# Optimization experiments

Hardware: AMD Instinct MI355X
Metric: run time of the kernel (lower is better)

## Reference

```python
import jax, jax.numpy as jnp
import numpy as np

IN, H, NCLS = 1280, 128, 263


def _lstm_scan(x_tbd, Wih, Whh, bih, bhh):
    # x_tbd: [T, B, IN]; PyTorch gate order: i, f, g, o. Wih: [4H, IN], Whh: [4H, H]
    B = x_tbd.shape[1]
    b = bih + bhh
    # precompute input projections once: [T, B, 4H]
    xp = jnp.einsum('tbd,gd->tbg', x_tbd, Wih) + b

    def step(carry, xg):
        h, c = carry
        gates = xg + h @ Whh.T
        i, f, g, o = jnp.split(gates, 4, axis=-1)
        i = jax.nn.sigmoid(i)
        f = jax.nn.sigmoid(f)
        g = jnp.tanh(g)
        o = jax.nn.sigmoid(o)
        c = f * c + i * g
        h = o * jnp.tanh(c)
        return (h, c), h

    h0 = jnp.zeros((B, H), x_tbd.dtype)
    c0 = jnp.zeros((B, H), x_tbd.dtype)
    _, hs = jax.lax.scan(step, (h0, c0), xp)
    return hs  # [T, B, H]


def setup_inputs() -> dict:
    key = jax.random.key(0)
    ks = jax.random.split(key, 11)
    s_ih = 1.0 / np.sqrt(H)
    u = lambda k, shape: jax.random.uniform(k, shape, jnp.float32, -s_ih, s_ih)
    return {
        'x': jax.random.normal(ks[0], (64, 512, IN), jnp.float32),
        'Wih_f': u(ks[1], (4 * H, IN)),
        'Whh_f': u(ks[2], (4 * H, H)),
        'bih_f': u(ks[3], (4 * H,)),
        'bhh_f': u(ks[4], (4 * H,)),
        'Wih_b': u(ks[5], (4 * H, IN)),
        'Whh_b': u(ks[6], (4 * H, H)),
        'bih_b': u(ks[7], (4 * H,)),
        'bhh_b': u(ks[8], (4 * H,)),
        'W1': u(ks[9], (NCLS, 2 * H)),
        'b1': u(ks[10], (NCLS,)),
    }


def reference(x, Wih_f, Whh_f, bih_f, bhh_f, Wih_b, Whh_b, bih_b, bhh_b, W1, b1):
    x_tbd = jnp.swapaxes(x, 0, 1)  # [T, B, IN]
    h_f = _lstm_scan(x_tbd, Wih_f, Whh_f, bih_f, bhh_f)           # [T, B, H]
    h_b = _lstm_scan(x_tbd[::-1], Wih_b, Whh_b, bih_b, bhh_b)[::-1]
    h = jnp.concatenate([h_f, h_b], axis=-1)  # [T, B, 2H]
    pooled = jnp.max(h, axis=0)               # temporal max-pool -> [B, 2H]
    # dropout treated as identity (deterministic eval-mode baseline)
    return pooled @ W1.T + b1                  # [B, 263]
```

## Files before the change

kernel.cpp:

```cpp
#include <hip/hip_runtime.h>
#include <hip/hip_bf16.h>

typedef short short8v __attribute__((ext_vector_type(8)));
typedef short short4v __attribute__((ext_vector_type(4)));
typedef float f32x4v __attribute__((ext_vector_type(4)));

#define T_LEN 512
#define BATCH 64
#define INDIM 1280
#define HDIM 128
#define G4 512
#define NCOLS 1024
#define NCLS 263

typedef __attribute__((address_space(1))) const void gvoid_t;
typedef __attribute__((address_space(3))) void lvoid_t;
#define GLOAD_LDS16(g, l) __builtin_amdgcn_global_load_lds((gvoid_t*)(g), (lvoid_t*)(l), 16, 0, 0)

static __device__ __forceinline__ short f2bf(float f) {
    union { float f; unsigned u; } v; v.f = f;
    unsigned r = v.u + 0x7FFF + ((v.u >> 16) & 1);
    return (short)(r >> 16);
}

__global__ void convert_x_kernel(const float4* __restrict__ x, short4v* __restrict__ out, int n4) {
    int i = blockIdx.x * blockDim.x + threadIdx.x;
    int stride = gridDim.x * blockDim.x;
    for (; i < n4; i += stride) {
        float4 v = x[i];
        short4v o;
        o[0] = f2bf(v.x); o[1] = f2bf(v.y); o[2] = f2bf(v.z); o[3] = f2bf(v.w);
        out[i] = o;
    }
}

__global__ void convert_w_kernel(const float* __restrict__ Wf, const float* __restrict__ Wb,
                                 const float* __restrict__ bihf, const float* __restrict__ bhhf,
                                 const float* __restrict__ bihb, const float* __restrict__ bhhb,
                                 short* __restrict__ wout, float* __restrict__ biasc) {
    int i = blockIdx.x * blockDim.x + threadIdx.x;
    int stride = gridDim.x * blockDim.x;
    const int n4 = (G4 * INDIM) / 4;
    for (int k = i; k < 2 * n4; k += stride) {
        const float4* src = (k < n4) ? (const float4*)Wf : (const float4*)Wb;
        float4 v = src[(k < n4) ? k : (k - n4)];
        short4v o;
        o[0] = f2bf(v.x); o[1] = f2bf(v.y); o[2] = f2bf(v.z); o[3] = f2bf(v.w);
        ((short4v*)wout)[k] = o;
    }
    if (i < NCOLS)
        biasc[i] = (i < G4) ? (bihf[i] + bhhf[i]) : (bihb[i - G4] + bhhb[i - G4]);
}

#define BM 128
#define BN 128
#define BK 32

__global__ __launch_bounds__(256) void gemm_xp_kernel(const short* __restrict__ A,
                                                      const short* __restrict__ Bw,
                                                      const float* __restrict__ bias,
                                                      float* __restrict__ C) {
    __shared__ __align__(16) short As[BM * BK];
    __shared__ __align__(16) short Bs[BN * BK];
    const int tid = threadIdx.x;
    const int w = tid >> 6;
    const int l = tid & 63;
    const int bm = blockIdx.x * BM;
    const int bn = blockIdx.y * BN;
    const int wm = (w >> 1) * 64;
    const int wn = (w & 1) * 64;
    const int lr = l & 15;
    const int lk = (l >> 4) * 8;

    f32x4v acc[4][4];
#pragma unroll
    for (int m = 0; m < 4; m++)
#pragma unroll
        for (int n = 0; n < 4; n++) acc[m][n] = (f32x4v)0.0f;

    const int srow = tid >> 2;
    const int scol = (tid & 3) * 8;

#pragma unroll
    for (int i = 0; i < 2; i++) {
        GLOAD_LDS16(A + (long)(bm + i * 64 + srow) * INDIM + scol, &As[(i * 64 + (w << 4)) * BK]);
        GLOAD_LDS16(Bw + (long)(bn + i * 64 + srow) * INDIM + scol, &Bs[(i * 64 + (w << 4)) * BK]);
    }

    for (int k0 = 0; k0 < INDIM; k0 += BK) {
        __syncthreads();
        short8v af[4], bf[4];
#pragma unroll
        for (int m = 0; m < 4; m++) af[m] = *(const short8v*)&As[(wm + m * 16 + lr) * BK + lk];
#pragma unroll
        for (int n = 0; n < 4; n++) bf[n] = *(const short8v*)&Bs[(wn + n * 16 + lr) * BK + lk];
        __syncthreads();
        if (k0 + BK < INDIM) {
            const int k1 = k0 + BK;
#pragma unroll
            for (int i = 0; i < 2; i++) {
                GLOAD_LDS16(A + (long)(bm + i * 64 + srow) * INDIM + k1 + scol, &As[(i * 64 + (w << 4)) * BK]);
                GLOAD_LDS16(Bw + (long)(bn + i * 64 + srow) * INDIM + k1 + scol, &Bs[(i * 64 + (w << 4)) * BK]);
            }
        }
#pragma unroll
        for (int m = 0; m < 4; m++)
#pragma unroll
            for (int n = 0; n < 4; n++)
                acc[m][n] = __builtin_amdgcn_mfma_f32_16x16x32_bf16(af[m], bf[n], acc[m][n], 0, 0, 0);
    }

#pragma unroll
    for (int m = 0; m < 4; m++) {
        const int row = bm + wm + m * 16 + (l >> 4) * 4;
#pragma unroll
        for (int n = 0; n < 4; n++) {
            const int col = bn + wn + n * 16 + lr;
            const float bv = bias[col];
#pragma unroll
            for (int r = 0; r < 4; r++)
                C[(long)(row + r) * NCOLS + col] = acc[m][n][r] + bv;
        }
    }
}

__global__ __launch_bounds__(256, 1) void lstm_rec_kernel(const float* __restrict__ xp,
                                                          const float* __restrict__ Whh_f,
                                                          const float* __restrict__ Whh_b,
                                                          float* __restrict__ pooled) {
    __shared__ __align__(16) short hbf[2][3][136];
    __shared__ __align__(16) float glds[4][2][136];

    const int bid = blockIdx.x;
    const int d = bid & 1;
    const int b0 = (bid >> 1) * 2;
    const int tid = threadIdx.x;
    const int w = tid >> 6;
    const int l = tid & 63;
    const int lr = l & 15;
    const int lg = l >> 4;
    const int lk = lg * 8;
    const int hrow = lr < 2 ? lr : 2;

    const float* __restrict__ Whh = d ? Whh_b : Whh_f;

    short8v afragW[8][4];
#pragma unroll
    for (int nt = 0; nt < 8; nt++) {
        const int gc = w * 128 + nt * 16 + lr;
#pragma unroll
        for (int kk = 0; kk < 4; kk++) {
            const float* src = Whh + gc * HDIM + kk * 32 + lk;
            short8v f;
#pragma unroll
            for (int j = 0; j < 8; j++) f[j] = f2bf(src[j]);
            afragW[nt][kk] = f;
        }
    }

    for (int i = tid; i < 2 * 3 * 136; i += 256) ((short*)hbf)[i] = 0;

    const int eb = tid >> 7;
    const int ec = tid & 127;
    const float* xbase = xp + (long)(b0 + eb) * T_LEN * NCOLS + d * G4 + ec;

    float c = 0.0f;
    float hmax = -1e30f;

#define LOADXV(tq, dst) { \
    int tt_ = d ? (T_LEN - 1 - (tq)) : (tq); \
    tt_ = tt_ < 0 ? 0 : (tt_ > T_LEN - 1 ? T_LEN - 1 : tt_); \
    const float* p_ = xbase + (long)tt_ * NCOLS; \
    _Pragma("unroll") for (int nt_ = 0; nt_ < 4; nt_++) \
        dst[nt_] = p_[nt_ * 128]; \
}

    float xvA[4], xvB[4];
    LOADXV(0, xvA);
    LOADXV(1, xvB);

    __syncthreads();

#define L2E 1.44269504088896f

#define STEP(t, pb, xv) { \
    short8v hfrag[4]; \
    _Pragma("unroll") for (int kk = 0; kk < 4; kk++) \
        hfrag[kk] = *(const short8v*)&hbf[pb][hrow][kk * 32 + lk]; \
    _Pragma("unroll") for (int nt = 0; nt < 8; nt++) { \
        f32x4v a = (f32x4v)0.0f; \
        _Pragma("unroll") for (int kk = 0; kk < 4; kk++) \
            a = __builtin_amdgcn_mfma_f32_16x16x32_bf16(afragW[nt][kk], hfrag[kk], a, 0, 0, 0); \
        if (lr < 2) *(f32x4v*)&glds[w][lr][nt * 16 + lg * 4] = a; \
    } \
    asm volatile("s_waitcnt lgkmcnt(0)\n\ts_barrier" ::: "memory"); \
    { \
        float gi = glds[0][eb][ec] + xv[0]; \
        float gf = glds[1][eb][ec] + xv[1]; \
        float gg = glds[2][eb][ec] + xv[2]; \
        float go = glds[3][eb][ec] + xv[3]; \
        float ea = __builtin_amdgcn_exp2f(-gi * L2E); \
        float eb_ = __builtin_amdgcn_exp2f(-gf * L2E); \
        float pa = 1.0f + ea, pbv = 1.0f + eb_; \
        float inv1 = __builtin_amdgcn_rcpf(pa * pbv); \
        float si = pbv * inv1; \
        float sf = pa * inv1; \
        float eg = __builtin_amdgcn_exp2f(gg * (2.0f * L2E)); \
        float eo = __builtin_amdgcn_exp2f(-go * L2E); \
        float pg = 1.0f + eg, po = 1.0f + eo; \
        float inv2 = __builtin_amdgcn_rcpf(pg * po); \
        float tg = 1.0f - 2.0f * po * inv2; \
        float so = pg * inv2; \
        c = sf * c + si * tg; \
        float ecx = __builtin_amdgcn_exp2f(c * (2.0f * L2E)); \
        float tc = 1.0f - 2.0f * __builtin_amdgcn_rcpf(1.0f + ecx); \
        float h = so * tc; \
        hmax = fmaxf(hmax, h); \
        hbf[(pb) ^ 1][eb][ec] = f2bf(h); \
    } \
    LOADXV((t) + 2, xv); \
    asm volatile("s_waitcnt lgkmcnt(0)\n\ts_barrier" ::: "memory"); \
}

    for (int t = 0; t < T_LEN; t += 2) {
        STEP(t, 0, xvA);
        STEP(t + 1, 1, xvB);
    }

    pooled[(b0 + eb) * 256 + d * 128 + ec] = hmax;
#undef STEP
#undef LOADXV
}

__global__ void logits_kernel(const float* __restrict__ pooled, const float* __restrict__ W1,
                              const float* __restrict__ b1, float* __restrict__ out) {
    __shared__ float p[256];
    const int b = blockIdx.x;
    const int n = threadIdx.x;
    if (n < 256) p[n] = pooled[b * 256 + n];
    __syncthreads();
    if (n < NCLS) {
        float s = b1[n];
        const float* wr = W1 + n * 256;
#pragma unroll 8
        for (int k = 0; k < 256; k++) s += p[k] * wr[k];
        out[b * NCLS + n] = s;
    }
}

extern "C" void kernel_launch(void* const* d_in, const int* in_sizes, int n_in,
                              void* d_out, int out_size, void* d_ws, size_t ws_size,
                              hipStream_t stream) {
    (void)in_sizes; (void)n_in; (void)out_size; (void)ws_size;
    const float* x     = (const float*)d_in[0];
    const float* Wih_f = (const float*)d_in[1];
    const float* Whh_f = (const float*)d_in[2];
    const float* bih_f = (const float*)d_in[3];
    const float* bhh_f = (const float*)d_in[4];
    const float* Wih_b = (const float*)d_in[5];
    const float* Whh_b = (const float*)d_in[6];
    const float* bih_b = (const float*)d_in[7];
    const float* bhh_b = (const float*)d_in[8];
    const float* W1    = (const float*)d_in[9];
    const float* b1    = (const float*)d_in[10];
    float* out = (float*)d_out;

    char* ws = (char*)d_ws;
    short* x_bf   = (short*)ws;
    short* w_bf   = (short*)(ws + 83886080);
    float* biasc  = (float*)(ws + 86507520);
    float* xp     = (float*)(ws + 86511616);
    float* pooled = (float*)(ws + 220729344);

    convert_x_kernel<<<2048, 256, 0, stream>>>((const float4*)x, (short4v*)x_bf, (T_LEN * BATCH * INDIM) / 4);
    convert_w_kernel<<<512, 256, 0, stream>>>(Wih_f, Wih_b, bih_f, bhh_f, bih_b, bhh_b, w_bf, biasc);
    dim3 g(BATCH * T_LEN / BM, NCOLS / BN);
    gemm_xp_kernel<<<g, 256, 0, stream>>>(x_bf, w_bf, biasc, xp);
    lstm_rec_kernel<<<64, 256, 0, stream>>>(xp, Whh_f, Whh_b, pooled);
    logits_kernel<<<64, 320, 0, stream>>>(pooled, W1, b1, out);
}
```

Before: 504.6 us.

## Double GEMM K-tile to 64 and remap blocks for XCD-aware L2 reuse

The input-projection GEMM's K tile grows from 32 to 64, which halves the number of k-iterations and barriers and issues twice as many MFMAs per LDS stage. The launch becomes a 1D grid of 2048 blocks, remapped so that consecutive logical tiles (the 8 N-tiles sharing an A row-block) land on the same XCD and can share A in L2. The LDS footprint doubles to 32KB, and per-thread registers grow from staging pointers and the doubled fragments. The GEMM is only part of the total pipeline, whose time is likely dominated by the recurrent LSTM kernel.

```diff
diff --git a/kernel.cpp b/kernel.cpp
--- a/kernel.cpp
+++ b/kernel.cpp
@@ -54,7 +54,8 @@
 
 #define BM 128
 #define BN 128
-#define BK 32
+#define BK 64
+#define GBLK 2048
 
 __global__ __launch_bounds__(256) void gemm_xp_kernel(const short* __restrict__ A,
                                                       const short* __restrict__ Bw,
@@ -65,8 +66,12 @@
     const int tid = threadIdx.x;
     const int w = tid >> 6;
     const int l = tid & 63;
-    const int bm = blockIdx.x * BM;
-    const int bn = blockIdx.y * BN;
+
+    const int orig = blockIdx.x;
+    const int logical = (orig & 7) * (GBLK / 8) + (orig >> 3);
+    const int bn = (logical & 7) * BN;
+    const int bm = (logical >> 3) * BM;
+
     const int wm = (w >> 1) * 64;
     const int wn = (w & 1) * 64;
     const int lr = l & 15;
@@ -78,36 +83,48 @@
 #pragma unroll
         for (int n = 0; n < 4; n++) acc[m][n] = (f32x4v)0.0f;
 
-    const int srow = tid >> 2;
-    const int scol = (tid & 3) * 8;
-
-#pragma unroll
-    for (int i = 0; i < 2; i++) {
-        GLOAD_LDS16(A + (long)(bm + i * 64 + srow) * INDIM + scol, &As[(i * 64 + (w << 4)) * BK]);
-        GLOAD_LDS16(Bw + (long)(bn + i * 64 + srow) * INDIM + scol, &Bs[(i * 64 + (w << 4)) * BK]);
-    }
+    const short* aptr[4];
+    const short* bptr[4];
+#pragma unroll
+    for (int c = 0; c < 4; c++) {
+        const int chunk = c * 256 + tid;
+        const int row = chunk >> 3;
+        const int col = (chunk & 7) * 8;
+        aptr[c] = A + (long)(bm + row) * INDIM + col;
+        bptr[c] = Bw + (long)(bn + row) * INDIM + col;
+    }
+
+#define STAGEK(k0) { \
+    _Pragma("unroll") for (int c_ = 0; c_ < 4; c_++) \
+        GLOAD_LDS16(aptr[c_] + (k0), &As[(c_ * 256 + w * 64) * 8]); \
+    _Pragma("unroll") for (int c_ = 0; c_ < 4; c_++) \
+        GLOAD_LDS16(bptr[c_] + (k0), &Bs[(c_ * 256 + w * 64) * 8]); \
+}
+
+    STAGEK(0);
 
     for (int k0 = 0; k0 < INDIM; k0 += BK) {
         __syncthreads();
-        short8v af[4], bf[4];
-#pragma unroll
-        for (int m = 0; m < 4; m++) af[m] = *(const short8v*)&As[(wm + m * 16 + lr) * BK + lk];
-#pragma unroll
-        for (int n = 0; n < 4; n++) bf[n] = *(const short8v*)&Bs[(wn + n * 16 + lr) * BK + lk];
+        short8v af[4][2], bf[4][2];
+#pragma unroll
+        for (int m = 0; m < 4; m++)
+#pragma unroll
+            for (int ks = 0; ks < 2; ks++)
+                af[m][ks] = *(const short8v*)&As[(wm + m * 16 + lr) * BK + ks * 32 + lk];
+#pragma unroll
+        for (int n = 0; n < 4; n++)
+#pragma unroll
+            for (int ks = 0; ks < 2; ks++)
+                bf[n][ks] = *(const short8v*)&Bs[(wn + n * 16 + lr) * BK + ks * 32 + lk];
         __syncthreads();
-        if (k0 + BK < INDIM) {
-            const int k1 = k0 + BK;
-#pragma unroll
-            for (int i = 0; i < 2; i++) {
-                GLOAD_LDS16(A + (long)(bm + i * 64 + srow) * INDIM + k1 + scol, &As[(i * 64 + (w << 4)) * BK]);
-                GLOAD_LDS16(Bw + (long)(bn + i * 64 + srow) * INDIM + k1 + scol, &Bs[(i * 64 + (w << 4)) * BK]);
-            }
-        }
-#pragma unroll
-        for (int m = 0; m < 4; m++)
-#pragma unroll
-            for (int n = 0; n < 4; n++)
-                acc[m][n] = __builtin_amdgcn_mfma_f32_16x16x32_bf16(af[m], bf[n], acc[m][n], 0, 0, 0);
+        if (k0 + BK < INDIM) STAGEK(k0 + BK);
+#pragma unroll
+        for (int ks = 0; ks < 2; ks++)
+#pragma unroll
+            for (int m = 0; m < 4; m++)
+#pragma unroll
+                for (int n = 0; n < 4; n++)
+                    acc[m][n] = __builtin_amdgcn_mfma_f32_16x16x32_bf16(af[m][ks], bf[n][ks], acc[m][n], 0, 0, 0);
     }
 
 #pragma unroll
@@ -122,6 +139,7 @@
                 C[(long)(row + r) * NCOLS + col] = acc[m][n][r] + bv;
         }
     }
+#undef STAGEK
 }
 
 __global__ __launch_bounds__(256, 1) void lstm_rec_kernel(const float* __restrict__ xp,
@@ -274,8 +292,7 @@
 
     convert_x_kernel<<<2048, 256, 0, stream>>>((const float4*)x, (short4v*)x_bf, (T_LEN * BATCH * INDIM) / 4);
     convert_w_kernel<<<512, 256, 0, stream>>>(Wih_f, Wih_b, bih_f, bhh_f, bih_b, bhh_b, w_bf, biasc);
-    dim3 g(BATCH * T_LEN / BM, NCOLS / BN);
-    gemm_xp_kernel<<<g, 256, 0, stream>>>(x_bf, w_bf, biasc, xp);
+    gemm_xp_kernel<<<GBLK, 256, 0, stream>>>(x_bf, w_bf, biasc, xp);
     lstm_rec_kernel<<<64, 256, 0, stream>>>(xp, Whh_f, Whh_b, pooled);
     logits_kernel<<<64, 320, 0, stream>>>(pooled, W1, b1, out);
 }
```

New measurement: 508.4 us. About the same (+0.8%).
